# Optimization experiments

Measured on AMD Instinct MI355X. Metric: run time of the kernel, lower is better.

The kernel has to match this reference:

```python
import jax, jax.numpy as jnp
import numpy as np
import math

B, N, H = 32, 512, 512  # batch, nodes_num (=input_dim), hidden_dim; upscale=1.0 -> d_qk = H


def setup_inputs() -> dict:
    key = jax.random.key(0)
    ks = jax.random.split(key, 4)
    s = 1.0 / math.sqrt(H)
    x = jax.random.normal(ks[0], (B, N, H), dtype=jnp.float32)
    Wq = jax.random.normal(ks[1], (H, H), dtype=jnp.float32) * s
    Wk = jax.random.normal(ks[2], (H, H), dtype=jnp.float32) * s
    Wm = jax.random.normal(ks[3], (N * H, H), dtype=jnp.float32) * (1.0 / math.sqrt(N * H))
    return {
        "x": x,
        "Wq": Wq, "bq": jnp.zeros((H,), jnp.float32),
        "Wk": Wk, "bk": jnp.zeros((H,), jnp.float32),
        "Wm": Wm, "bm": jnp.zeros((H,), jnp.float32),
    }


def reference(x, Wq, bq, Wk, bk, Wm, bm):
    # q/k projections (Linear stored as (in, out))
    q = jnp.einsum('bnh,hd->bnd', x, Wq) + bq          # [B,N,D]
    k = jnp.einsum('bnh,hd->bnd', x, Wk) + bk          # [B,N,D]
    d = q.shape[-1]
    scores = jnp.einsum('bnd,bmd->bnm', q, k) / math.sqrt(d)
    attention = jax.nn.softmax(jax.nn.sigmoid(scores), axis=-1)  # [B,N,N]
    out = jnp.einsum('bnm,bmh->bnh', attention, x)     # dropout = identity (eval)
    b, n, h = x.shape
    out = out.reshape(b, n * h) @ Wm + bm              # [B,H]
    return (out, attention)
```

## Files before the change

kernel.cpp:

```cpp
#include <hip/hip_runtime.h>

#define BB 32
#define NN 512
#define HH 512
constexpr float QK_SCALE = 0.04419417382415922f;

using bf16x8 = __attribute__((ext_vector_type(8))) short;
using f32x4  = __attribute__((ext_vector_type(4))) float;
typedef unsigned int u32;

__device__ __forceinline__ short f2bf(float f) {
  unsigned int u = __float_as_uint(f);
  unsigned int r = (u + 0x7FFFu + ((u >> 16) & 1u)) >> 16;
  return (short)r;
}

__device__ __forceinline__ void gl_lds16(const short* g, short* l) {
  __builtin_amdgcn_global_load_lds(
      (const __attribute__((address_space(1))) u32*)g,
      (__attribute__((address_space(3))) u32*)l, 16, 0, 0);
}

__global__ __launch_bounds__(256) void prep_x(const float* __restrict__ x,
                                              short* __restrict__ xbf,
                                              short* __restrict__ xT) {
  __shared__ float tile[32][33];
  const int b = blockIdx.z;
  const int n0 = blockIdx.y * 32, h0 = blockIdx.x * 32;
  const int t = threadIdx.x;
  const int i = t >> 3;
  const int j4 = (t & 7) * 4;
  const float4 v = *(const float4*)&x[((long)b * NN + n0 + i) * HH + h0 + j4];
  short o[4] = {f2bf(v.x), f2bf(v.y), f2bf(v.z), f2bf(v.w)};
  *(uint2*)&xbf[((long)b * NN + n0 + i) * HH + h0 + j4] = *(uint2*)o;
  tile[i][j4 + 0] = v.x; tile[i][j4 + 1] = v.y;
  tile[i][j4 + 2] = v.z; tile[i][j4 + 3] = v.w;
  __syncthreads();
  short p[4] = {f2bf(tile[j4 + 0][i]), f2bf(tile[j4 + 1][i]),
                f2bf(tile[j4 + 2][i]), f2bf(tile[j4 + 3][i])};
  *(uint2*)&xT[((long)b * HH + h0 + i) * NN + n0 + j4] = *(uint2*)p;
}

__global__ __launch_bounds__(256) void prep_w(const float* __restrict__ Wq,
                                              const float* __restrict__ Wk,
                                              short* __restrict__ Wqt,
                                              short* __restrict__ Wkt) {
  __shared__ float tile[32][33];
  const float* W = blockIdx.z ? Wk : Wq;
  short* Wt = blockIdx.z ? Wkt : Wqt;
  const int h0 = blockIdx.y * 32, d0 = blockIdx.x * 32;
  const int t = threadIdx.x;
  const int i = t >> 3;
  const int j4 = (t & 7) * 4;
  const float4 v = *(const float4*)&W[(long)(h0 + i) * HH + d0 + j4];
  tile[i][j4 + 0] = v.x; tile[i][j4 + 1] = v.y;
  tile[i][j4 + 2] = v.z; tile[i][j4 + 3] = v.w;
  __syncthreads();
  short p[4] = {f2bf(tile[j4 + 0][i]), f2bf(tile[j4 + 1][i]),
                f2bf(tile[j4 + 2][i]), f2bf(tile[j4 + 3][i])};
  *(uint2*)&Wt[(long)(d0 + i) * HH + h0 + j4] = *(uint2*)p;
}

template <int WRITE_BF16>
__global__ __launch_bounds__(256) void gemm128(const short* __restrict__ A,
                                               const short* __restrict__ Bt,
                                               void* __restrict__ Cv,
                                               const float* __restrict__ bias,
                                               float scale, int M, int Nc, int K,
                                               long sA, long sB, long sC) {
  __shared__ short As[128 * 64];
  __shared__ short Bs[128 * 64];
  A  += (long)blockIdx.z * sA;
  Bt += (long)blockIdx.z * sB;
  const int m0 = blockIdx.x * 128;
  const int n0 = blockIdx.y * 128;
  const int t = threadIdx.x;
  const int wave = t >> 6, lane = t & 63;
  const int lrow = lane & 15, lq = lane >> 4;
  const int wr = (wave >> 1) * 64, wc = (wave & 1) * 64;

  const int srow = t >> 3;
  const int scol = (t & 7) * 8;
  const short* Ag = A  + (long)(m0 + srow) * K + scol;
  const short* Bg = Bt + (long)(n0 + srow) * K + scol;
  short* Al = &As[srow * 64 + scol];
  short* Bl = &Bs[srow * 64 + scol];
  const long gstep = (long)32 * K;

  f32x4 acc[4][4] = {};
  for (int k0 = 0; k0 < K; k0 += 64) {
#pragma unroll
    for (int p = 0; p < 4; ++p) {
      gl_lds16(Ag + k0 + p * gstep, Al + p * 32 * 64);
      gl_lds16(Bg + k0 + p * gstep, Bl + p * 32 * 64);
    }
    __syncthreads();
#pragma unroll
    for (int kk = 0; kk < 64; kk += 32) {
      bf16x8 a[4], b[4];
#pragma unroll
      for (int i = 0; i < 4; ++i) {
        a[i] = *(const bf16x8*)&As[(wr + i * 16 + lrow) * 64 + kk + lq * 8];
        b[i] = *(const bf16x8*)&Bs[(wc + i * 16 + lrow) * 64 + kk + lq * 8];
      }
#pragma unroll
      for (int m = 0; m < 4; ++m)
#pragma unroll
        for (int n = 0; n < 4; ++n)
          acc[m][n] = __builtin_amdgcn_mfma_f32_16x16x32_bf16(a[m], b[n], acc[m][n], 0, 0, 0);
    }
    __syncthreads();
  }

  const long cb = (long)blockIdx.z * sC;
#pragma unroll
  for (int m = 0; m < 4; ++m) {
#pragma unroll
    for (int r = 0; r < 4; ++r) {
      const long row = m0 + wr + m * 16 + lq * 4 + r;
#pragma unroll
      for (int n = 0; n < 4; ++n) {
        const int col = n0 + wc + n * 16 + lrow;
        float v = acc[m][n][r] * scale;
        if (bias) v += bias[col];
        if (WRITE_BF16)
          ((short*)Cv)[cb + row * Nc + col] = f2bf(v);
        else
          ((float*)Cv)[cb + row * Nc + col] = v;
      }
    }
  }
}

__global__ __launch_bounds__(256) void sigsoftmax(float* __restrict__ att,
                                                  short* __restrict__ attbf) {
  const long row = blockIdx.x;
  float* p = att + row * NN;
  const int t = threadIdx.x;
  float2 v = *(float2*)&p[t * 2];
  const float s0 = 1.f / (1.f + __expf(-v.x));
  const float s1 = 1.f / (1.f + __expf(-v.y));
  const float e0 = __expf(s0), e1 = __expf(s1);
  float sum = e0 + e1;
#pragma unroll
  for (int o = 32; o > 0; o >>= 1) sum += __shfl_down(sum, o);
  __shared__ float wsum[4];
  if ((t & 63) == 0) wsum[t >> 6] = sum;
  __syncthreads();
  const float r = 1.f / (wsum[0] + wsum[1] + wsum[2] + wsum[3]);
  const float a0 = e0 * r, a1 = e1 * r;
  float2 o2; o2.x = a0; o2.y = a1;
  *(float2*)&p[t * 2] = o2;
  short pk[2] = {f2bf(a0), f2bf(a1)};
  *(unsigned int*)&attbf[row * NN + t * 2] = *(unsigned int*)pk;
}

__global__ __launch_bounds__(256) void gemm_final(const short* __restrict__ A,
                                                  const float* __restrict__ Wm,
                                                  float* __restrict__ part) {
  __shared__ short As[32 * 72];
  __shared__ short Bs[64 * 72];
  const int j0 = blockIdx.y * 64;
  const long KT = (long)NN * HH;
  const long Kc = KT / gridDim.x;
  const long i0b = (long)blockIdx.x * Kc;
  const int t = threadIdx.x;
  const int wave = t >> 6, lane = t & 63;
  const int lrow = lane & 15, lq = lane >> 4;
  const int ar = t >> 3, ac = (t & 7) * 8;
  const int kr = t >> 4, jc = (t & 15) * 4;
  f32x4 acc[2] = {};
  for (long i0 = i0b; i0 < i0b + Kc; i0 += 64) {
    *(uint4*)&As[ar * 72 + ac] = *(const uint4*)&A[(long)ar * KT + i0 + ac];
#pragma unroll
    for (int p = 0; p < 4; ++p) {
      const float4 w = *(const float4*)&Wm[(i0 + kr + p * 16) * HH + j0 + jc];
      Bs[(jc + 0) * 72 + kr + p * 16] = f2bf(w.x);
      Bs[(jc + 1) * 72 + kr + p * 16] = f2bf(w.y);
      Bs[(jc + 2) * 72 + kr + p * 16] = f2bf(w.z);
      Bs[(jc + 3) * 72 + kr + p * 16] = f2bf(w.w);
    }
    __syncthreads();
#pragma unroll
    for (int kk = 0; kk < 64; kk += 32) {
      bf16x8 b  = *(const bf16x8*)&Bs[(wave * 16 + lrow) * 72 + kk + lq * 8];
      bf16x8 a0 = *(const bf16x8*)&As[lrow * 72 + kk + lq * 8];
      bf16x8 a1 = *(const bf16x8*)&As[(16 + lrow) * 72 + kk + lq * 8];
      acc[0] = __builtin_amdgcn_mfma_f32_16x16x32_bf16(a0, b, acc[0], 0, 0, 0);
      acc[1] = __builtin_amdgcn_mfma_f32_16x16x32_bf16(a1, b, acc[1], 0, 0, 0);
    }
    __syncthreads();
  }
  float* dst = part + (long)blockIdx.x * (BB * HH);
#pragma unroll
  for (int mt = 0; mt < 2; ++mt)
#pragma unroll
    for (int r = 0; r < 4; ++r) {
      const int row = mt * 16 + lq * 4 + r;
      const int col = j0 + wave * 16 + lrow;
      dst[(long)row * HH + col] = acc[mt][r];
    }
}

__global__ __launch_bounds__(256) void reduce_out(const float* __restrict__ part,
                                                  const float* __restrict__ bm,
                                                  float* __restrict__ out) {
  const int idx = blockIdx.x * 256 + threadIdx.x;
  float s0 = bm[idx & (HH - 1)], s1 = 0.f, s2 = 0.f, s3 = 0.f;
#pragma unroll 8
  for (int p = 0; p < 128; p += 4) {
    s0 += part[(long)(p + 0) * (BB * HH) + idx];
    s1 += part[(long)(p + 1) * (BB * HH) + idx];
    s2 += part[(long)(p + 2) * (BB * HH) + idx];
    s3 += part[(long)(p + 3) * (BB * HH) + idx];
  }
  out[idx] = (s0 + s1) + (s2 + s3);
}

extern "C" void kernel_launch(void* const* d_in, const int* in_sizes, int n_in,
                              void* d_out, int out_size, void* d_ws, size_t ws_size,
                              hipStream_t stream) {
  const float* x  = (const float*)d_in[0];
  const float* Wq = (const float*)d_in[1];
  const float* bq = (const float*)d_in[2];
  const float* Wk = (const float*)d_in[3];
  const float* bk = (const float*)d_in[4];
  const float* Wm = (const float*)d_in[5];
  const float* bm = (const float*)d_in[6];
  float* out = (float*)d_out;
  float* att = out + (long)BB * HH;

  char* ws = (char*)d_ws;
  const long SZ = (long)BB * NN * HH * sizeof(short);
  short* buf0 = (short*)ws;
  short* buf1 = (short*)(ws + SZ);
  short* buf2 = (short*)(ws + 2 * SZ);
  short* buf3 = (short*)(ws + 3 * SZ);
  short* wqt  = (short*)(ws + 4 * SZ);
  short* wkt  = wqt + (long)HH * HH;
  float* part = (float*)buf3;

  prep_x<<<dim3(HH / 32, NN / 32, BB), 256, 0, stream>>>(x, buf0, buf1);
  prep_w<<<dim3(HH / 32, HH / 32, 2), 256, 0, stream>>>(Wq, Wk, wqt, wkt);

  gemm128<1><<<dim3(BB * NN / 128, HH / 128, 1), 256, 0, stream>>>(
      buf0, wqt, buf2, bq, 1.f, BB * NN, HH, HH, 0, 0, 0);
  gemm128<1><<<dim3(BB * NN / 128, HH / 128, 1), 256, 0, stream>>>(
      buf0, wkt, buf3, bk, 1.f, BB * NN, HH, HH, 0, 0, 0);

  gemm128<0><<<dim3(NN / 128, NN / 128, BB), 256, 0, stream>>>(
      buf2, buf3, att, nullptr, QK_SCALE, NN, NN, HH,
      (long)NN * HH, (long)NN * HH, (long)NN * NN);

  sigsoftmax<<<dim3(BB * NN), 256, 0, stream>>>(att, buf2);

  gemm128<1><<<dim3(NN / 128, HH / 128, BB), 256, 0, stream>>>(
      buf2, buf1, buf0, nullptr, 1.f, NN, HH, NN,
      (long)NN * NN, (long)HH * NN, (long)NN * HH);

  gemm_final<<<dim3(128, HH / 64, 1), 256, 0, stream>>>(buf0, Wm, part);
  reduce_out<<<dim3(BB * HH / 256), 256, 0, stream>>>(part, bm, out);
}
```

Baseline: 841.4 us.

## Fuse QK^T with sigmoid-softmax and merge prep and projection launches

```diff
diff --git a/kernel.cpp b/kernel.cpp
--- a/kernel.cpp
+++ b/kernel.cpp
@@ -21,56 +21,184 @@
       (__attribute__((address_space(3))) u32*)l, 16, 0, 0);
 }
 
-__global__ __launch_bounds__(256) void prep_x(const float* __restrict__ x,
-                                              short* __restrict__ xbf,
-                                              short* __restrict__ xT) {
+__global__ __launch_bounds__(256) void prep_all(const float* __restrict__ x,
+                                                short* __restrict__ xbf,
+                                                short* __restrict__ xT,
+                                                const float* __restrict__ Wq,
+                                                const float* __restrict__ Wk,
+                                                short* __restrict__ Wqt,
+                                                short* __restrict__ Wkt) {
   __shared__ float tile[32][33];
-  const int b = blockIdx.z;
-  const int n0 = blockIdx.y * 32, h0 = blockIdx.x * 32;
+  const int bid = blockIdx.x;
   const int t = threadIdx.x;
   const int i = t >> 3;
   const int j4 = (t & 7) * 4;
-  const float4 v = *(const float4*)&x[((long)b * NN + n0 + i) * HH + h0 + j4];
-  short o[4] = {f2bf(v.x), f2bf(v.y), f2bf(v.z), f2bf(v.w)};
-  *(uint2*)&xbf[((long)b * NN + n0 + i) * HH + h0 + j4] = *(uint2*)o;
-  tile[i][j4 + 0] = v.x; tile[i][j4 + 1] = v.y;
-  tile[i][j4 + 2] = v.z; tile[i][j4 + 3] = v.w;
-  __syncthreads();
-  short p[4] = {f2bf(tile[j4 + 0][i]), f2bf(tile[j4 + 1][i]),
-                f2bf(tile[j4 + 2][i]), f2bf(tile[j4 + 3][i])};
-  *(uint2*)&xT[((long)b * HH + h0 + i) * NN + n0 + j4] = *(uint2*)p;
-}
-
-__global__ __launch_bounds__(256) void prep_w(const float* __restrict__ Wq,
-                                              const float* __restrict__ Wk,
-                                              short* __restrict__ Wqt,
-                                              short* __restrict__ Wkt) {
-  __shared__ float tile[32][33];
-  const float* W = blockIdx.z ? Wk : Wq;
-  short* Wt = blockIdx.z ? Wkt : Wqt;
-  const int h0 = blockIdx.y * 32, d0 = blockIdx.x * 32;
-  const int t = threadIdx.x;
-  const int i = t >> 3;
-  const int j4 = (t & 7) * 4;
-  const float4 v = *(const float4*)&W[(long)(h0 + i) * HH + d0 + j4];
-  tile[i][j4 + 0] = v.x; tile[i][j4 + 1] = v.y;
-  tile[i][j4 + 2] = v.z; tile[i][j4 + 3] = v.w;
-  __syncthreads();
-  short p[4] = {f2bf(tile[j4 + 0][i]), f2bf(tile[j4 + 1][i]),
-                f2bf(tile[j4 + 2][i]), f2bf(tile[j4 + 3][i])};
-  *(uint2*)&Wt[(long)(d0 + i) * HH + h0 + j4] = *(uint2*)p;
-}
-
-template <int WRITE_BF16>
+  if (bid < 8192) {
+    const int b = bid >> 8;
+    const int n0 = ((bid >> 4) & 15) * 32, h0 = (bid & 15) * 32;
+    const float4 v = *(const float4*)&x[((long)b * NN + n0 + i) * HH + h0 + j4];
+    short o[4] = {f2bf(v.x), f2bf(v.y), f2bf(v.z), f2bf(v.w)};
+    *(uint2*)&xbf[((long)b * NN + n0 + i) * HH + h0 + j4] = *(uint2*)o;
+    tile[i][j4 + 0] = v.x; tile[i][j4 + 1] = v.y;
+    tile[i][j4 + 2] = v.z; tile[i][j4 + 3] = v.w;
+    __syncthreads();
+    short p[4] = {f2bf(tile[j4 + 0][i]), f2bf(tile[j4 + 1][i]),
+                  f2bf(tile[j4 + 2][i]), f2bf(tile[j4 + 3][i])};
+    *(uint2*)&xT[((long)b * HH + h0 + i) * NN + n0 + j4] = *(uint2*)p;
+  } else {
+    const int id = bid - 8192;
+    const float* W = (id >> 8) ? Wk : Wq;
+    short* Wt = (id >> 8) ? Wkt : Wqt;
+    const int h0 = ((id >> 4) & 15) * 32, d0 = (id & 15) * 32;
+    const float4 v = *(const float4*)&W[(long)(h0 + i) * HH + d0 + j4];
+    tile[i][j4 + 0] = v.x; tile[i][j4 + 1] = v.y;
+    tile[i][j4 + 2] = v.z; tile[i][j4 + 3] = v.w;
+    __syncthreads();
+    short p[4] = {f2bf(tile[j4 + 0][i]), f2bf(tile[j4 + 1][i]),
+                  f2bf(tile[j4 + 2][i]), f2bf(tile[j4 + 3][i])};
+    *(uint2*)&Wt[(long)(d0 + i) * HH + h0 + j4] = *(uint2*)p;
+  }
+}
+
+__global__ __launch_bounds__(256) void gemm_qk(const short* __restrict__ A,
+                                               const short* __restrict__ Wt_pair,
+                                               short* __restrict__ Cq,
+                                               short* __restrict__ Ck,
+                                               const float* __restrict__ bq,
+                                               const float* __restrict__ bk) {
+  __shared__ short As[128 * 64];
+  __shared__ short Bs[128 * 64];
+  const short* Bt = Wt_pair + (long)blockIdx.z * HH * HH;
+  short* C = blockIdx.z ? Ck : Cq;
+  const float* bias = blockIdx.z ? bk : bq;
+  const int m0 = blockIdx.x * 128;
+  const int n0 = blockIdx.y * 128;
+  const int t = threadIdx.x;
+  const int wave = t >> 6, lane = t & 63;
+  const int lrow = lane & 15, lq = lane >> 4;
+  const int wr = (wave >> 1) * 64, wc = (wave & 1) * 64;
+
+  const int srow = t >> 3;
+  const int scol = (t & 7) * 8;
+  const short* Ag = A + (long)(m0 + srow) * HH + scol;
+  const short* Bg = Bt + (long)(n0 + srow) * HH + scol;
+  short* Al = &As[srow * 64 + scol];
+  short* Bl = &Bs[srow * 64 + scol];
+  const long gstep = (long)32 * HH;
+
+  f32x4 acc[4][4] = {};
+  for (int k0 = 0; k0 < HH; k0 += 64) {
+#pragma unroll
+    for (int p = 0; p < 4; ++p) {
+      gl_lds16(Ag + k0 + p * gstep, Al + p * 32 * 64);
+      gl_lds16(Bg + k0 + p * gstep, Bl + p * 32 * 64);
+    }
+    __syncthreads();
+#pragma unroll
+    for (int kk = 0; kk < 64; kk += 32) {
+      bf16x8 a[4], b[4];
+#pragma unroll
+      for (int i = 0; i < 4; ++i) {
+        a[i] = *(const bf16x8*)&As[(wr + i * 16 + lrow) * 64 + kk + lq * 8];
+        b[i] = *(const bf16x8*)&Bs[(wc + i * 16 + lrow) * 64 + kk + lq * 8];
+      }
+#pragma unroll
+      for (int m = 0; m < 4; ++m)
+#pragma unroll
+        for (int n = 0; n < 4; ++n)
+          acc[m][n] = __builtin_amdgcn_mfma_f32_16x16x32_bf16(a[m], b[n], acc[m][n], 0, 0, 0);
+    }
+    __syncthreads();
+  }
+
+#pragma unroll
+  for (int m = 0; m < 4; ++m)
+#pragma unroll
+    for (int r = 0; r < 4; ++r) {
+      const long row = m0 + wr + m * 16 + lq * 4 + r;
+#pragma unroll
+      for (int n = 0; n < 4; ++n) {
+        const int col = n0 + wc + n * 16 + lrow;
+        C[row * HH + col] = f2bf(acc[m][n][r] + bias[col]);
+      }
+    }
+}
+
+__global__ __launch_bounds__(256) void gemm_ssm(const short* q,
+                                                short* attbf,
+                                                const short* __restrict__ k,
+                                                float* __restrict__ att) {
+  __shared__ short Qs[64 * 32];
+  __shared__ short Ks[512 * 32];
+  const int b = blockIdx.y;
+  const int r0 = blockIdx.x * 64;
+  const int t = threadIdx.x;
+  const int wave = t >> 6, lane = t & 63;
+  const int lrow = lane & 15, lq = lane >> 4;
+
+  const short* qg = q + ((long)b * NN + r0 + (t >> 2)) * HH + (t & 3) * 8;
+  short* ql = &Qs[t * 8];
+  const short* kg = k + ((long)b * NN + (t >> 2)) * HH + (t & 3) * 8;
+  short* kl = &Ks[t * 8];
+
+  f32x4 acc[32];
+#pragma unroll
+  for (int i = 0; i < 32; ++i) acc[i] = (f32x4){0.f, 0.f, 0.f, 0.f};
+
+  for (int k0 = 0; k0 < HH; k0 += 32) {
+    gl_lds16(qg + k0, ql);
+#pragma unroll
+    for (int p = 0; p < 8; ++p)
+      gl_lds16(kg + k0 + (long)p * 64 * HH, kl + p * 2048);
+    __syncthreads();
+    const bf16x8 a = *(const bf16x8*)&Qs[(wave * 16 + lrow) * 32 + lq * 8];
+#pragma unroll
+    for (int nt = 0; nt < 32; ++nt) {
+      const bf16x8 bb = *(const bf16x8*)&Ks[(nt * 16 + lrow) * 32 + lq * 8];
+      acc[nt] = __builtin_amdgcn_mfma_f32_16x16x32_bf16(a, bb, acc[nt], 0, 0, 0);
+    }
+    __syncthreads();
+  }
+
+  float rs[4] = {0.f, 0.f, 0.f, 0.f};
+#pragma unroll
+  for (int nt = 0; nt < 32; ++nt)
+#pragma unroll
+    for (int r = 0; r < 4; ++r) {
+      const float s = acc[nt][r] * QK_SCALE;
+      const float sg = 1.f / (1.f + __expf(-s));
+      const float ev = __expf(sg);
+      acc[nt][r] = ev;
+      rs[r] += ev;
+    }
+#pragma unroll
+  for (int r = 0; r < 4; ++r) {
+    rs[r] += __shfl_xor(rs[r], 1);
+    rs[r] += __shfl_xor(rs[r], 2);
+    rs[r] += __shfl_xor(rs[r], 4);
+    rs[r] += __shfl_xor(rs[r], 8);
+    rs[r] = 1.f / rs[r];
+  }
+  const int row0 = r0 + wave * 16 + lq * 4;
+#pragma unroll
+  for (int nt = 0; nt < 32; ++nt)
+#pragma unroll
+    for (int r = 0; r < 4; ++r) {
+      const float av = acc[nt][r] * rs[r];
+      const long idx = ((long)b * NN + row0 + r) * NN + nt * 16 + lrow;
+      att[idx] = av;
+      attbf[idx] = f2bf(av);
+    }
+}
+
 __global__ __launch_bounds__(256) void gemm128(const short* __restrict__ A,
                                                const short* __restrict__ Bt,
-                                               void* __restrict__ Cv,
-                                               const float* __restrict__ bias,
-                                               float scale, int M, int Nc, int K,
+                                               short* __restrict__ C,
+                                               int Nc, int K,
                                                long sA, long sB, long sC) {
   __shared__ short As[128 * 64];
   __shared__ short Bs[128 * 64];
-  A  += (long)blockIdx.z * sA;
+  A += (long)blockIdx.z * sA;
   Bt += (long)blockIdx.z * sB;
   const int m0 = blockIdx.x * 128;
   const int n0 = blockIdx.y * 128;
@@ -78,10 +206,9 @@
   const int wave = t >> 6, lane = t & 63;
   const int lrow = lane & 15, lq = lane >> 4;
   const int wr = (wave >> 1) * 64, wc = (wave & 1) * 64;
-
   const int srow = t >> 3;
   const int scol = (t & 7) * 8;
-  const short* Ag = A  + (long)(m0 + srow) * K + scol;
+  const short* Ag = A + (long)(m0 + srow) * K + scol;
   const short* Bg = Bt + (long)(n0 + srow) * K + scol;
   short* Al = &As[srow * 64 + scol];
   short* Bl = &Bs[srow * 64 + scol];
@@ -114,45 +241,16 @@
 
   const long cb = (long)blockIdx.z * sC;
 #pragma unroll
-  for (int m = 0; m < 4; ++m) {
+  for (int m = 0; m < 4; ++m)
 #pragma unroll
     for (int r = 0; r < 4; ++r) {
       const long row = m0 + wr + m * 16 + lq * 4 + r;
 #pragma unroll
       for (int n = 0; n < 4; ++n) {
         const int col = n0 + wc + n * 16 + lrow;
-        float v = acc[m][n][r] * scale;
-        if (bias) v += bias[col];
-        if (WRITE_BF16)
-          ((short*)Cv)[cb + row * Nc + col] = f2bf(v);
-        else
-          ((float*)Cv)[cb + row * Nc + col] = v;
+        C[cb + row * Nc + col] = f2bf(acc[m][n][r]);
       }
     }
-  }
-}
-
-__global__ __launch_bounds__(256) void sigsoftmax(float* __restrict__ att,
-                                                  short* __restrict__ attbf) {
-  const long row = blockIdx.x;
-  float* p = att + row * NN;
-  const int t = threadIdx.x;
-  float2 v = *(float2*)&p[t * 2];
-  const float s0 = 1.f / (1.f + __expf(-v.x));
-  const float s1 = 1.f / (1.f + __expf(-v.y));
-  const float e0 = __expf(s0), e1 = __expf(s1);
-  float sum = e0 + e1;
-#pragma unroll
-  for (int o = 32; o > 0; o >>= 1) sum += __shfl_down(sum, o);
-  __shared__ float wsum[4];
-  if ((t & 63) == 0) wsum[t >> 6] = sum;
-  __syncthreads();
-  const float r = 1.f / (wsum[0] + wsum[1] + wsum[2] + wsum[3]);
-  const float a0 = e0 * r, a1 = e1 * r;
-  float2 o2; o2.x = a0; o2.y = a1;
-  *(float2*)&p[t * 2] = o2;
-  short pk[2] = {f2bf(a0), f2bf(a1)};
-  *(unsigned int*)&attbf[row * NN + t * 2] = *(unsigned int*)pk;
 }
 
 __global__ __launch_bounds__(256) void gemm_final(const short* __restrict__ A,
@@ -240,22 +338,15 @@
   short* wkt  = wqt + (long)HH * HH;
   float* part = (float*)buf3;
 
-  prep_x<<<dim3(HH / 32, NN / 32, BB), 256, 0, stream>>>(x, buf0, buf1);
-  prep_w<<<dim3(HH / 32, HH / 32, 2), 256, 0, stream>>>(Wq, Wk, wqt, wkt);
-
-  gemm128<1><<<dim3(BB * NN / 128, HH / 128, 1), 256, 0, stream>>>(
-      buf0, wqt, buf2, bq, 1.f, BB * NN, HH, HH, 0, 0, 0);
-  gemm128<1><<<dim3(BB * NN / 128, HH / 128, 1), 256, 0, stream>>>(
-      buf0, wkt, buf3, bk, 1.f, BB * NN, HH, HH, 0, 0, 0);
-
-  gemm128<0><<<dim3(NN / 128, NN / 128, BB), 256, 0, stream>>>(
-      buf2, buf3, att, nullptr, QK_SCALE, NN, NN, HH,
-      (long)NN * HH, (long)NN * HH, (long)NN * NN);
-
-  sigsoftmax<<<dim3(BB * NN), 256, 0, stream>>>(att, buf2);
-
-  gemm128<1><<<dim3(NN / 128, HH / 128, BB), 256, 0, stream>>>(
-      buf2, buf1, buf0, nullptr, 1.f, NN, HH, NN,
+  prep_all<<<dim3(8192 + 512), 256, 0, stream>>>(x, buf0, buf1, Wq, Wk, wqt, wkt);
+
+  gemm_qk<<<dim3(BB * NN / 128, HH / 128, 2), 256, 0, stream>>>(
+      buf0, wqt, buf2, buf3, bq, bk);
+
+  gemm_ssm<<<dim3(NN / 64, BB), 256, 0, stream>>>(buf2, buf2, buf3, att);
+
+  gemm128<<<dim3(NN / 128, HH / 128, BB), 256, 0, stream>>>(
+      buf2, buf1, buf0, HH, NN,
       (long)NN * NN, (long)HH * NN, (long)NN * HH);
 
   gemm_final<<<dim3(128, HH / 64, 1), 256, 0, stream>>>(buf0, Wm, part);
```

Result: no change. 834.2 us (-0.9%).
